# Kernel optimization log

Measured on AMD Instinct MI355X. Metric: run time of the kernel, lower is better.

## Reference

```python
import jax, jax.numpy as jnp
import numpy as np

N, E, IN, OUT = 50000, 800000, 128, 128
R = 5  # num_rels + 1 (last slice is the self-loop weight)


def setup_inputs() -> dict:
    key = jax.random.key(0)
    k = jax.random.split(key, 6)
    x = jax.random.normal(k[0], (N, IN), jnp.float32)
    src = jax.random.randint(k[1], (E,), 0, N)
    dst = jax.random.randint(k[2], (E,), 0, N)
    rel = jax.random.randint(k[3], (E,), 0, R - 1)  # edge rel_type in [0, num_rels)
    xavier = np.sqrt(2.0) * np.sqrt(6.0 / (IN + OUT))  # gain('relu') * xavier bound scale
    weight = jax.random.uniform(k[4], (R, IN, OUT), jnp.float32, -xavier, xavier)
    bias = jax.random.uniform(k[5], (R, OUT), jnp.float32, -xavier, xavier)
    return dict(x=x, weight=weight, bias=bias, src=src, dst=dst, rel=rel)


def reference(x, weight, bias, src, dst, rel):
    num_nodes = x.shape[0]
    num_edge_rels = weight.shape[0] - 1
    x_src = x[src]  # [E, IN] per-edge source gather
    # Per-edge message: x_src @ weight[rel] + bias[rel].
    # Grouped-GEMM style: one dense GEMM per relation, select by mask
    # (avoids materializing [E, IN, OUT] per-edge weights).
    msg = jnp.zeros((src.shape[0], weight.shape[2]), x.dtype)
    for r in range(num_edge_rels):
        hr = x_src @ weight[r] + bias[r]  # [E, OUT]
        msg = jnp.where((rel == r)[:, None], hr, msg)
    # Max-aggregation onto destination nodes; DGL fills 0 for nodes w/o in-edges.
    agg = jax.ops.segment_max(msg, dst, num_segments=num_nodes)  # [N, OUT]
    deg = jax.ops.segment_sum(jnp.ones_like(dst, jnp.float32), dst, num_segments=num_nodes)
    agg = jnp.where((deg > 0)[:, None], agg, jnp.zeros((), x.dtype))
    # Self-loop transform with last weight/bias slice.
    h = x @ weight[-1] + bias[-1] + agg
    return h
```

## Files before the change

kernel.cpp:

```cpp
#include <hip/hip_runtime.h>

#define NNODES 50000
#define NEDGES 800000
#define DIM    128
#define NRELS  4
#define NBLK2  25
#define DBLK   128
#define NDB    (4*DBLK)
#define NFB    3125
#define EPB    12500
#define NHC    64
#define RNG    25000
#define NPB    782

typedef __attribute__((ext_vector_type(8))) short bf16x8;
typedef __attribute__((ext_vector_type(8))) unsigned short u16x8;
typedef __attribute__((ext_vector_type(4))) float f32x4;

#define SSRC_OFF 0
#define CNT_OFF  3200000
#define BSUM_OFF 3404800
#define RANK_OFF 3405056
#define PCNT_OFF 5005056
#define WT_OFF   11405056
#define XBF_OFF  11568896
#define H_OFF    24368896

__device__ __forceinline__ unsigned short f2bf(float f) {
  unsigned u = __float_as_uint(f);
  return (unsigned short)((u + 0x7FFFu + ((u >> 16) & 1u)) >> 16);
}

__global__ __launch_bounds__(1024) void k_ph(
    const float* __restrict__ x, unsigned short* __restrict__ xbf,
    const float* __restrict__ W, unsigned short* __restrict__ Wt,
    const int* __restrict__ dst, unsigned short* __restrict__ rank,
    unsigned short* __restrict__ pcnt) {
  __shared__ unsigned lh[RNG / 2];
  if (blockIdx.x < NHC * 2) {
    int c = blockIdx.x >> 1;
    int r0 = (blockIdx.x & 1) * RNG;
    for (int i = threadIdx.x; i < RNG / 2; i += 1024) lh[i] = 0u;
    __syncthreads();
    int e0 = c * EPB;
    for (int e = e0 + threadIdx.x; e < e0 + EPB; e += 1024) {
      int d = dst[e] - r0;
      if ((unsigned)d < (unsigned)RNG) {
        unsigned old = atomicAdd(&lh[d >> 1], (d & 1) ? 65536u : 1u);
        rank[e] = (unsigned short)((old >> ((d & 1) << 4)) & 0xFFFFu);
      }
    }
    __syncthreads();
    unsigned* prow = (unsigned*)(pcnt + (size_t)c * NNODES + r0);
    for (int i = threadIdx.x; i < RNG / 2; i += 1024) prow[i] = lh[i];
    return;
  }
  int i = (blockIdx.x - NHC * 2) * 1024 + threadIdx.x;
  if (i < NNODES * DIM / 8) {
    const float4* p = (const float4*)x + i * 2;
    float4 v0 = p[0], v1 = p[1];
    u16x8 o;
    o[0] = f2bf(v0.x); o[1] = f2bf(v0.y); o[2] = f2bf(v0.z); o[3] = f2bf(v0.w);
    o[4] = f2bf(v1.x); o[5] = f2bf(v1.y); o[6] = f2bf(v1.z); o[7] = f2bf(v1.w);
    *(u16x8*)(xbf + i * 8) = o;
  }
  if (i < 5 * DIM * DIM) {
    int r = i >> 14, rem = i & 16383, k = rem >> 7, c = rem & 127;
    Wt[(r << 14) + (c << 7) + k] = f2bf(W[i]);
  }
}

__global__ void k_scanC(unsigned short* __restrict__ pcnt, unsigned* __restrict__ cnt) {
  int d = blockIdx.x * 256 + threadIdx.x;
  if (d < NNODES) {
    unsigned run = 0;
#pragma unroll 8
    for (int b = 0; b < NHC; b++) {
      size_t off = (size_t)b * NNODES + d;
      unsigned v = pcnt[off];
      pcnt[off] = (unsigned short)run;
      run += v;
    }
    cnt[d] = run;
  } else {
    cnt[d] = 0;
  }
}

__global__ void k_scanA(unsigned* __restrict__ cnt, unsigned* __restrict__ bsum) {
  __shared__ unsigned sh[256];
  int tid = threadIdx.x;
  int base = blockIdx.x * 2048 + tid * 8;
  unsigned v[8], tsum = 0;
#pragma unroll
  for (int j = 0; j < 8; j++) { v[j] = cnt[base + j]; tsum += v[j]; }
  sh[tid] = tsum;
  __syncthreads();
  for (int off = 1; off < 256; off <<= 1) {
    unsigned t = (tid >= off) ? sh[tid - off] : 0u;
    __syncthreads();
    sh[tid] += t;
    __syncthreads();
  }
  unsigned run = sh[tid] - tsum;
#pragma unroll
  for (int j = 0; j < 8; j++) { unsigned t = v[j]; cnt[base + j] = run; run += t; }
  if (tid == 255) bsum[blockIdx.x] = sh[255];
}

__global__ void k_fix(unsigned* __restrict__ cnt, const unsigned* __restrict__ bsum) {
  int blk = blockIdx.x;
  if (blk == 0) return;
  unsigned p = 0;
  for (int k = 0; k < blk; k++) p += bsum[k];
  int base = blk * 2048 + threadIdx.x * 8;
#pragma unroll
  for (int j = 0; j < 8; j++) cnt[base + j] += p;
}

__global__ __launch_bounds__(256, 2) void k_dfill(
    const unsigned short* __restrict__ xbf, const unsigned short* __restrict__ Wt,
    const float* __restrict__ bias, unsigned short* __restrict__ H,
    const int* __restrict__ rel, const int* __restrict__ dst,
    const int* __restrict__ src, const unsigned* __restrict__ cnt,
    const unsigned short* __restrict__ rank, const unsigned short* __restrict__ pfx,
    unsigned* __restrict__ ssrc) {
  if (blockIdx.x >= NDB) {
    int e = (blockIdx.x - NDB) * 256 + threadIdx.x;
    if (e < NEDGES) {
      int r = rel[e]; r = r < 0 ? 0 : (r > NRELS - 1 ? NRELS - 1 : r);
      int d = dst[e];
      unsigned pos = cnt[d] + (unsigned)pfx[(size_t)(e / EPB) * NNODES + d] + (unsigned)rank[e];
      ssrc[pos] = (unsigned)(r * NNODES + src[e]);
    }
    return;
  }
  __shared__ unsigned short st[4][2048];
  int lane = threadIdx.x & 63;
  int wv = threadIdx.x >> 6;
  int r = blockIdx.x / DBLK;
  const int NT = NNODES / 16;
  int col = lane & 15, quad = lane >> 4;

  const unsigned short* wr = Wt + (r << 14);
  bf16x8 B[8][4];
  float bs[8];
#pragma unroll
  for (int ct = 0; ct < 8; ct++) {
#pragma unroll
    for (int kk = 0; kk < 4; kk++)
      B[ct][kk] = *(const bf16x8*)(wr + ((ct * 16 + col) << 7) + kk * 32 + quad * 8);
    bs[ct] = bias[(r << 7) + ct * 16 + col];
  }

  for (int t = (blockIdx.x % DBLK) * 4 + wv; t < NT; t += DBLK * 4) {
    int n0 = t * 16;
    int na = n0 + col;
    bf16x8 a0 = *(const bf16x8*)(xbf + (na << 7) + quad * 8);
    bf16x8 a1 = *(const bf16x8*)(xbf + (na << 7) + 32 + quad * 8);
    bf16x8 a2 = *(const bf16x8*)(xbf + (na << 7) + 64 + quad * 8);
    bf16x8 a3 = *(const bf16x8*)(xbf + (na << 7) + 96 + quad * 8);

#pragma unroll
    for (int ct = 0; ct < 8; ct++) {
      f32x4 acc = {0.f, 0.f, 0.f, 0.f};
      acc = __builtin_amdgcn_mfma_f32_16x16x32_bf16(a0, B[ct][0], acc, 0, 0, 0);
      acc = __builtin_amdgcn_mfma_f32_16x16x32_bf16(a1, B[ct][1], acc, 0, 0, 0);
      acc = __builtin_amdgcn_mfma_f32_16x16x32_bf16(a2, B[ct][2], acc, 0, 0, 0);
      acc = __builtin_amdgcn_mfma_f32_16x16x32_bf16(a3, B[ct][3], acc, 0, 0, 0);
      int cc = ct * 16 + col;
#pragma unroll
      for (int j = 0; j < 4; j++) st[wv][(quad * 4 + j) * 128 + cc] = f2bf(acc[j] + bs[ct]);
    }
    unsigned short* gb = H + (((size_t)(r * NNODES + n0)) << 7);
#pragma unroll
    for (int s = 0; s < 4; s++) {
      int off = s * 512 + lane * 8;
      *(u16x8*)(gb + off) = *(const u16x8*)(&st[wv][off]);
    }
  }
}

__global__ __launch_bounds__(256, 8) void k_agg(
    const unsigned* __restrict__ cnt, const unsigned* __restrict__ ssrc,
    const uint4* __restrict__ H4, const unsigned short* __restrict__ xbf,
    const unsigned short* __restrict__ Wt, const float* __restrict__ bias,
    float* __restrict__ out) {
  __shared__ float smax[16][128];
  int tid = threadIdx.x;
  int n0 = blockIdx.x * 16;

  int lane16 = tid & 15;
  int q = tid >> 4;
  int n = n0 + q;
  unsigned base = cnt[n];
  int deg = (int)(cnt[n + 1] - base);
  float init = (deg > 0) ? -3.0e38f : 0.0f;
  float m0 = init, m1 = init, m2 = init, m3 = init;
  float m4 = init, m5 = init, m6 = init, m7 = init;
#define UNP(v)                                          \
  m0 = fmaxf(m0, __uint_as_float((v).x << 16));         \
  m1 = fmaxf(m1, __uint_as_float((v).x & 0xFFFF0000u)); \
  m2 = fmaxf(m2, __uint_as_float((v).y << 16));         \
  m3 = fmaxf(m3, __uint_as_float((v).y & 0xFFFF0000u)); \
  m4 = fmaxf(m4, __uint_as_float((v).z << 16));         \
  m5 = fmaxf(m5, __uint_as_float((v).z & 0xFFFF0000u)); \
  m6 = fmaxf(m6, __uint_as_float((v).w << 16));         \
  m7 = fmaxf(m7, __uint_as_float((v).w & 0xFFFF0000u))
  if (deg > 0) {
    int lim = deg - 1;
    for (int i = 0; i < deg; i += 8) {
      unsigned c0 = ssrc[base + min(i, lim)];
      unsigned c1 = ssrc[base + min(i + 1, lim)];
      unsigned c2 = ssrc[base + min(i + 2, lim)];
      unsigned c3 = ssrc[base + min(i + 3, lim)];
      unsigned c4 = ssrc[base + min(i + 4, lim)];
      unsigned c5 = ssrc[base + min(i + 5, lim)];
      unsigned c6 = ssrc[base + min(i + 6, lim)];
      unsigned c7 = ssrc[base + min(i + 7, lim)];
      uint4 v0 = H4[((size_t)c0 << 4) + lane16];
      uint4 v1 = H4[((size_t)c1 << 4) + lane16];
      uint4 v2 = H4[((size_t)c2 << 4) + lane16];
      uint4 v3 = H4[((size_t)c3 << 4) + lane16];
      uint4 v4 = H4[((size_t)c4 << 4) + lane16];
      uint4 v5 = H4[((size_t)c5 << 4) + lane16];
      uint4 v6 = H4[((size_t)c6 << 4) + lane16];
      uint4 v7 = H4[((size_t)c7 << 4) + lane16];
      UNP(v0); UNP(v1); UNP(v2); UNP(v3);
      UNP(v4); UNP(v5); UNP(v6); UNP(v7);
    }
  }
#undef UNP
  float4* sp = (float4*)&smax[q][lane16 * 8];
  sp[0] = (float4){m0, m1, m2, m3};
  sp[1] = (float4){m4, m5, m6, m7};
  __syncthreads();

  int l64 = tid & 63;
  int wv = tid >> 6;
  int col = l64 & 15, quad = l64 >> 4;
  const unsigned short* wr = Wt + (4 << 14);
  int na = n0 + col;
  bf16x8 a0 = *(const bf16x8*)(xbf + (na << 7) + quad * 8);
  bf16x8 a1 = *(const bf16x8*)(xbf + (na << 7) + 32 + quad * 8);
  bf16x8 a2 = *(const bf16x8*)(xbf + (na << 7) + 64 + quad * 8);
  bf16x8 a3 = *(const bf16x8*)(xbf + (na << 7) + 96 + quad * 8);
#pragma unroll
  for (int cti = 0; cti < 2; cti++) {
    int ct = wv * 2 + cti;
    bf16x8 b0 = *(const bf16x8*)(wr + ((ct * 16 + col) << 7) + 0 * 32 + quad * 8);
    bf16x8 b1 = *(const bf16x8*)(wr + ((ct * 16 + col) << 7) + 1 * 32 + quad * 8);
    bf16x8 b2 = *(const bf16x8*)(wr + ((ct * 16 + col) << 7) + 2 * 32 + quad * 8);
    bf16x8 b3 = *(const bf16x8*)(wr + ((ct * 16 + col) << 7) + 3 * 32 + quad * 8);
    float bsv = bias[(4 << 7) + ct * 16 + col];
    f32x4 acc = {0.f, 0.f, 0.f, 0.f};
    acc = __builtin_amdgcn_mfma_f32_16x16x32_bf16(a0, b0, acc, 0, 0, 0);
    acc = __builtin_amdgcn_mfma_f32_16x16x32_bf16(a1, b1, acc, 0, 0, 0);
    acc = __builtin_amdgcn_mfma_f32_16x16x32_bf16(a2, b2, acc, 0, 0, 0);
    acc = __builtin_amdgcn_mfma_f32_16x16x32_bf16(a3, b3, acc, 0, 0, 0);
    int cc = ct * 16 + col;
#pragma unroll
    for (int j = 0; j < 4; j++) {
      int row = quad * 4 + j;
      __builtin_nontemporal_store(acc[j] + bsv + smax[row][cc],
                                  out + ((size_t)(n0 + row) << 7) + (unsigned)cc);
    }
  }
}

extern "C" void kernel_launch(void* const* d_in, const int* in_sizes, int n_in,
                              void* d_out, int out_size, void* d_ws, size_t ws_size,
                              hipStream_t stream) {
  const float* x = (const float*)d_in[0];
  const float* W = (const float*)d_in[1];
  const float* bias = (const float*)d_in[2];
  const int* src = (const int*)d_in[3];
  const int* dst = (const int*)d_in[4];
  const int* rel = (const int*)d_in[5];

  char* ws = (char*)d_ws;
  unsigned* ssrc = (unsigned*)(ws + SSRC_OFF);
  unsigned* cnt = (unsigned*)(ws + CNT_OFF);
  unsigned* bsum = (unsigned*)(ws + BSUM_OFF);
  unsigned short* rank = (unsigned short*)(ws + RANK_OFF);
  unsigned short* pcnt = (unsigned short*)(ws + PCNT_OFF);
  unsigned short* Wt = (unsigned short*)(ws + WT_OFF);
  unsigned short* xbf = (unsigned short*)(ws + XBF_OFF);
  unsigned short* H = (unsigned short*)(ws + H_OFF);
  float* out = (float*)d_out;

  hipLaunchKernelGGL(k_ph, dim3(NHC * 2 + NPB), dim3(1024), 0, stream, x, xbf, W, Wt, dst, rank,
                     pcnt);
  hipLaunchKernelGGL(k_scanC, dim3(200), dim3(256), 0, stream, pcnt, cnt);
  hipLaunchKernelGGL(k_scanA, dim3(NBLK2), dim3(256), 0, stream, cnt, bsum);
  hipLaunchKernelGGL(k_fix, dim3(NBLK2), dim3(256), 0, stream, cnt, bsum);
  hipLaunchKernelGGL(k_dfill, dim3(NDB + NFB), dim3(256), 0, stream, xbf, Wt, bias, H, rel,
                     dst, src, cnt, rank, pcnt, ssrc);
  hipLaunchKernelGGL(k_agg, dim3(3125), dim3(256), 0, stream, cnt, ssrc, (const uint4*)H, xbf,
                     Wt, bias, out);
}
```

Before: 183.4 us.

## Fuse three scan kernels into one with a grid-wide spin barrier

```diff
diff --git a/kernel.cpp b/kernel.cpp
--- a/kernel.cpp
+++ b/kernel.cpp
@@ -4,7 +4,6 @@
 #define NEDGES 800000
 #define DIM    128
 #define NRELS  4
-#define NBLK2  25
 #define DBLK   128
 #define NDB    (4*DBLK)
 #define NFB    3125
@@ -12,6 +11,7 @@
 #define NHC    64
 #define RNG    25000
 #define NPB    782
+#define SCB    200
 
 typedef __attribute__((ext_vector_type(8))) short bf16x8;
 typedef __attribute__((ext_vector_type(8))) unsigned short u16x8;
@@ -20,11 +20,11 @@
 #define SSRC_OFF 0
 #define CNT_OFF  3200000
 #define BSUM_OFF 3404800
-#define RANK_OFF 3405056
-#define PCNT_OFF 5005056
-#define WT_OFF   11405056
-#define XBF_OFF  11568896
-#define H_OFF    24368896
+#define RANK_OFF 3405824
+#define PCNT_OFF 5005824
+#define WT_OFF   11405824
+#define XBF_OFF  11569664
+#define H_OFF    24369664
 
 __device__ __forceinline__ unsigned short f2bf(float f) {
   unsigned u = __float_as_uint(f);
@@ -35,9 +35,10 @@
     const float* __restrict__ x, unsigned short* __restrict__ xbf,
     const float* __restrict__ W, unsigned short* __restrict__ Wt,
     const int* __restrict__ dst, unsigned short* __restrict__ rank,
-    unsigned short* __restrict__ pcnt) {
+    unsigned short* __restrict__ pcnt, unsigned* flag) {
   __shared__ unsigned lh[RNG / 2];
   if (blockIdx.x < NHC * 2) {
+    if (blockIdx.x == 0 && threadIdx.x == 0) atomicExch(flag, 0u);
     int c = blockIdx.x >> 1;
     int r0 = (blockIdx.x & 1) * RNG;
     for (int i = threadIdx.x; i < RNG / 2; i += 1024) lh[i] = 0u;
@@ -70,10 +71,14 @@
   }
 }
 
-__global__ void k_scanC(unsigned short* __restrict__ pcnt, unsigned* __restrict__ cnt) {
-  int d = blockIdx.x * 256 + threadIdx.x;
+__global__ __launch_bounds__(256) void k_scan(unsigned short* __restrict__ pcnt,
+                                              unsigned* __restrict__ cnt,
+                                              unsigned* bsum, unsigned* flag) {
+  __shared__ unsigned sh[256];
+  int tid = threadIdx.x, blk = blockIdx.x;
+  int d = blk * 256 + tid;
+  unsigned run = 0;
   if (d < NNODES) {
-    unsigned run = 0;
 #pragma unroll 8
     for (int b = 0; b < NHC; b++) {
       size_t off = (size_t)b * NNODES + d;
@@ -81,20 +86,8 @@
       pcnt[off] = (unsigned short)run;
       run += v;
     }
-    cnt[d] = run;
-  } else {
-    cnt[d] = 0;
-  }
-}
-
-__global__ void k_scanA(unsigned* __restrict__ cnt, unsigned* __restrict__ bsum) {
-  __shared__ unsigned sh[256];
-  int tid = threadIdx.x;
-  int base = blockIdx.x * 2048 + tid * 8;
-  unsigned v[8], tsum = 0;
-#pragma unroll
-  for (int j = 0; j < 8; j++) { v[j] = cnt[base + j]; tsum += v[j]; }
-  sh[tid] = tsum;
+  }
+  sh[tid] = run;
   __syncthreads();
   for (int off = 1; off < 256; off <<= 1) {
     unsigned t = (tid >= off) ? sh[tid - off] : 0u;
@@ -102,20 +95,23 @@
     sh[tid] += t;
     __syncthreads();
   }
-  unsigned run = sh[tid] - tsum;
-#pragma unroll
-  for (int j = 0; j < 8; j++) { unsigned t = v[j]; cnt[base + j] = run; run += t; }
-  if (tid == 255) bsum[blockIdx.x] = sh[255];
-}
-
-__global__ void k_fix(unsigned* __restrict__ cnt, const unsigned* __restrict__ bsum) {
-  int blk = blockIdx.x;
-  if (blk == 0) return;
-  unsigned p = 0;
-  for (int k = 0; k < blk; k++) p += bsum[k];
-  int base = blk * 2048 + threadIdx.x * 8;
-#pragma unroll
-  for (int j = 0; j < 8; j++) cnt[base + j] += p;
+  unsigned excl = sh[tid] - run;
+  unsigned btot = sh[255];
+  __syncthreads();
+  if (tid == 0) {
+    atomicExch(&bsum[blk], btot);
+    atomicAdd(flag, 1u);
+    while (atomicAdd(flag, 0u) < SCB) { __builtin_amdgcn_s_sleep(8); }
+  }
+  __syncthreads();
+  unsigned pv = (tid < blk) ? atomicAdd(&bsum[tid], 0u) : 0u;
+  sh[tid] = pv;
+  __syncthreads();
+  for (int off = 128; off > 0; off >>= 1) {
+    if (tid < off) sh[tid] += sh[tid + off];
+    __syncthreads();
+  }
+  cnt[d] = sh[0] + excl;
 }
 
 __global__ __launch_bounds__(256, 2) void k_dfill(
@@ -282,6 +278,7 @@
   unsigned* ssrc = (unsigned*)(ws + SSRC_OFF);
   unsigned* cnt = (unsigned*)(ws + CNT_OFF);
   unsigned* bsum = (unsigned*)(ws + BSUM_OFF);
+  unsigned* flag = (unsigned*)(ws + BSUM_OFF + 800);
   unsigned short* rank = (unsigned short*)(ws + RANK_OFF);
   unsigned short* pcnt = (unsigned short*)(ws + PCNT_OFF);
   unsigned short* Wt = (unsigned short*)(ws + WT_OFF);
@@ -290,10 +287,8 @@
   float* out = (float*)d_out;
 
   hipLaunchKernelGGL(k_ph, dim3(NHC * 2 + NPB), dim3(1024), 0, stream, x, xbf, W, Wt, dst, rank,
-                     pcnt);
-  hipLaunchKernelGGL(k_scanC, dim3(200), dim3(256), 0, stream, pcnt, cnt);
-  hipLaunchKernelGGL(k_scanA, dim3(NBLK2), dim3(256), 0, stream, cnt, bsum);
-  hipLaunchKernelGGL(k_fix, dim3(NBLK2), dim3(256), 0, stream, cnt, bsum);
+                     pcnt, flag);
+  hipLaunchKernelGGL(k_scan, dim3(SCB), dim3(256), 0, stream, pcnt, cnt, bsum, flag);
   hipLaunchKernelGGL(k_dfill, dim3(NDB + NFB), dim3(256), 0, stream, xbf, Wt, bias, H, rel,
                      dst, src, cnt, rank, pcnt, ssrc);
   hipLaunchKernelGGL(k_agg, dim3(3125), dim3(256), 0, stream, cnt, ssrc, (const uint4*)H, xbf,
```

Result: no change. 184.8 us (+0.7%).
